# Kernel optimization log

Hardware: AMD Instinct MI355X
Metric: run time of the kernel (lower is better)

The kernel has to match this reference:

```python
import jax, jax.numpy as jnp
from jax import lax
import numpy as np

FEAT = 2048
HID = 512
OUT = 22
B, T = 16, 2048


def _kaiming(key, shape):
    fan_in = shape[1]
    std = np.sqrt(2.0 / fan_in)
    return jax.random.normal(key, shape, dtype=jnp.float32) * std


def setup_inputs() -> dict:
    key = jax.random.key(0)
    ks = jax.random.split(key, 12)
    x = jax.random.normal(ks[0], (B, T, FEAT), dtype=jnp.float32)
    inp = {
        "x": x,
        # main cell (PyTorch LSTMCell gate order: i, f, g, o)
        "w_ih": _kaiming(ks[1], (4 * HID, FEAT)),
        "w_hh": _kaiming(ks[2], (4 * HID, HID)),
        "b_ih": jax.random.uniform(ks[3], (4 * HID,), minval=-0.04, maxval=0.04),
        "b_hh": jax.random.uniform(ks[4], (4 * HID,), minval=-0.04, maxval=0.04),
        # ed cell
        "w_ih_ed": _kaiming(ks[5], (4 * HID, FEAT)),
        "w_hh_ed": _kaiming(ks[6], (4 * HID, HID)),
        "b_ih_ed": jax.random.uniform(ks[7], (4 * HID,), minval=-0.04, maxval=0.04),
        "b_hh_ed": jax.random.uniform(ks[8], (4 * HID,), minval=-0.04, maxval=0.04),
        # linear heads
        "fc_w": _kaiming(ks[9], (OUT, HID)),
        "fc_b": jnp.zeros((OUT,), dtype=jnp.float32),
        "fc_ed_w": _kaiming(ks[10], (OUT, HID)),
        "fc_ed_b": jnp.zeros((OUT,), dtype=jnp.float32),
    }
    return inp


def _run_lstm(x, w_ih, w_hh, b_ih, b_hh):
    # Precompute input projection for all timesteps: [B, T, 4H]
    xg = jnp.einsum("btf,gf->btg", x, w_ih) + (b_ih + b_hh)
    hid = w_hh.shape[1]
    b = x.shape[0]

    def step(carry, xg_t):
        h, c = carry
        g = xg_t + h @ w_hh.T  # [B, 4H]
        i, f, gg, o = jnp.split(g, 4, axis=-1)
        c = jax.nn.sigmoid(f) * c + jax.nn.sigmoid(i) * jnp.tanh(gg)
        h = jax.nn.sigmoid(o) * jnp.tanh(c)
        return (h, c), h

    init = (jnp.zeros((b, hid), x.dtype), jnp.zeros((b, hid), x.dtype))
    _, hs = lax.scan(step, init, jnp.swapaxes(xg, 0, 1))  # hs: [T, B, H]
    return jnp.swapaxes(hs, 0, 1)  # [B, T, H]


def reference(x, w_ih, w_hh, b_ih, b_hh, w_ih_ed, w_hh_ed, b_ih_ed, b_hh_ed,
              fc_w, fc_b, fc_ed_w, fc_ed_b):
    hs = _run_lstm(x, w_ih, w_hh, b_ih, b_hh)
    score = jnp.einsum("bth,oh->bto", hs, fc_w) + fc_b
    hs_ed = _run_lstm(x, w_ih_ed, w_hh_ed, b_ih_ed, b_hh_ed)
    ed = jnp.einsum("bth,oh->bto", hs_ed, fc_ed_w) + fc_ed_b
    return (score, ed)
```

## Files before the change

### kernel.cpp

```cpp
#include <hip/hip_runtime.h>
#include <hip/hip_bf16.h>
#include <stdint.h>

typedef __attribute__((ext_vector_type(8))) short s16x8;
typedef __attribute__((ext_vector_type(4))) float f32x4;
typedef unsigned short u16;
typedef unsigned int u32;
typedef unsigned long long u64;

#define FEAT 2048
#define HID  512
#define GATES 2048
#define NB   16
#define NT   2048
#define NOUT 22
#define MROWS (NB*NT)

#define WS_FLAG 0L
#define WS_BIAS 4096L
#define WS_WF   (WS_BIAS + 16384L)
#define WS_WB   (WS_WF + 4194304L)
#define WS_XB   (WS_WB + 16777216L)
#define WS_XG   (WS_XB + 134217728L)
#define WS_HB   (WS_XG + 268435456L)
#define HB_BYTES 67141632L
#define HB_LSTM_U64 (2049L*2048L)
#define HB_SLAB_U64 2048L

__device__ inline float b2f(u16 u){ u32 x = ((u32)u) << 16; return __builtin_bit_cast(float, x); }
__device__ inline u16 f2b(float f){
  u32 u = __builtin_bit_cast(u32, f);
  u32 r = (u + 0x7FFFu + ((u >> 16) & 1u)) >> 16;
  return (u16)r;
}
__device__ inline float sigm(float x){ return __builtin_amdgcn_rcpf(1.f + __expf(-x)); }
__device__ inline float tanh_(float x){ return 1.f - 2.f*__builtin_amdgcn_rcpf(1.f + __expf(2.f*x)); }

__global__ void detect_dtype(const u32* __restrict__ x, int* __restrict__ flag){
  __shared__ int cs;
  if (threadIdx.x == 0) cs = 0;
  __syncthreads();
  int c = 0;
  for (int i = 0; i < 16; i++){
    u32 w = x[threadIdx.x*16 + i];
    u32 e = (w >> 7) & 0xFFu;
    if ((e >= 110u && e <= 134u) || ((w & 0xFFFFu) == 0u)) c++;
  }
  atomicAdd(&cs, c);
  __syncthreads();
  if (threadIdx.x == 0) *flag = (cs > 2048) ? 1 : 0;
}

__global__ void cvt_bf16(const void* __restrict__ src, u16* __restrict__ dst,
                         long n8, const int* __restrict__ flag){
  const int isb = *flag;
  long stride = (long)gridDim.x * blockDim.x;
  for (long i = (long)blockIdx.x*blockDim.x + threadIdx.x; i < n8; i += stride){
    if (isb){
      ((int4*)dst)[i] = ((const int4*)src)[i];
    } else {
      const float4* s = (const float4*)src + 2*i;
      float4 a = s[0], b = s[1];
      s16x8 o;
      o[0]=(short)f2b(a.x); o[1]=(short)f2b(a.y); o[2]=(short)f2b(a.z); o[3]=(short)f2b(a.w);
      o[4]=(short)f2b(b.x); o[5]=(short)f2b(b.y); o[6]=(short)f2b(b.z); o[7]=(short)f2b(b.w);
      *(s16x8*)(dst + i*8) = o;
    }
  }
}

__global__ void bias_sum(const void* bi0, const void* bh0, const void* bi1, const void* bh1,
                         float* __restrict__ out, const int* __restrict__ flag){
  const int isb = *flag;
  int i = blockIdx.x*256 + threadIdx.x;
  int lstm = i >> 11, idx = i & 2047;
  const void* bi = lstm ? bi1 : bi0;
  const void* bh = lstm ? bh1 : bh0;
  float a = isb ? b2f(((const u16*)bi)[idx]) : ((const float*)bi)[idx];
  float b = isb ? b2f(((const u16*)bh)[idx]) : ((const float*)bh)[idx];
  out[i] = a + b;
}

__global__ void reorder_w(const void* __restrict__ w0, const void* __restrict__ w1,
                          u16* __restrict__ wfr, const int* __restrict__ flag){
  const int isb = *flag;
  int t = blockIdx.x*256 + threadIdx.x;
  int l   = t & 63;
  int kk  = (t >> 6) & 15;
  int tau = (t >> 10) & 127;
  int lstm = t >> 17;
  int m = tau >> 5;
  int w = tau & 31;
  int j = m*512 + w*16 + (l & 15);
  size_t sidx = (size_t)j*HID + kk*32 + (l >> 4)*8;
  const void* src = lstm ? w1 : w0;
  s16x8 o;
  if (isb){
    o = *(const s16x8*)((const u16*)src + sidx);
  } else {
    const float* s = (const float*)src + sidx;
#pragma unroll
    for (int e = 0; e < 8; e++) o[e] = (short)f2b(s[e]);
  }
  *(s16x8*)(wfr + ((((size_t)lstm*128 + tau)*16 + kk)*64 + l)*8) = o;
}

union FSmem {
  struct { u16 As[2][8192]; u16 Bs[2][8192]; } g;
  s16x8 Wl[4][16][64];
  char pad[102400];
};

__global__ __launch_bounds__(256,1) void fused_rec(const u16* __restrict__ wfr,
    const u16* __restrict__ xb, const u16* __restrict__ wb,
    const float* __restrict__ bias, u16* __restrict__ xg, u64* __restrict__ hb64){
  __shared__ FSmem sm;

  if (blockIdx.x >= 64){
    const int gid = blockIdx.x - 64;
    const int lstm = gid & 1;
    const int n0 = ((gid >> 1) & 15) * 128;
    const int y = gid >> 5;
    const int b = y & 15;
    const int tblk = y >> 4;
    const int m0 = b*NT + tblk*128;
    const int tid = threadIdx.x;
    const int lane = tid & 63;
    const int wid = tid >> 6;
    const int wr = wid >> 1, wc = wid & 1;
    const u16* Bw = wb + (size_t)lstm * GATES * FEAT;

    f32x4 acc[4][4] = {};

    auto stage = [&](int buf, int kt){
      const int k0 = kt*64;
#pragma unroll
      for (int i = 0; i < 4; i++){
        int cc = tid + 256*i;
        int row = cc >> 3;
        int slot = cc & 7;
        int slotp = slot ^ (row & 7);
        const u16* ga = xb + (size_t)(m0+row)*FEAT + k0 + slotp*8;
        const u16* gb = Bw + (size_t)(n0+row)*FEAT + k0 + slotp*8;
        __builtin_amdgcn_global_load_lds((const __attribute__((address_space(1))) void*)ga,
            (__attribute__((address_space(3))) void*)&sm.g.As[buf][cc*8], 16, 0, 0);
        __builtin_amdgcn_global_load_lds((const __attribute__((address_space(1))) void*)gb,
            (__attribute__((address_space(3))) void*)&sm.g.Bs[buf][cc*8], 16, 0, 0);
      }
    };

    stage(0, 0);
    __syncthreads();
    for (int kt = 0; kt < 32; kt++){
      int buf = kt & 1;
      if (kt < 31) stage(buf^1, kt+1);
      const char* Ab = (const char*)&sm.g.As[buf][0];
      const char* Bb = (const char*)&sm.g.Bs[buf][0];
#pragma unroll
      for (int ks = 0; ks < 2; ks++){
        s16x8 af[4], bf[4];
#pragma unroll
        for (int mi = 0; mi < 4; mi++){
          int row = wr*64 + mi*16 + (lane & 15);
          int off = row*128 + ((ks*64 + ((lane>>4)*16)) ^ ((row & 7) << 4));
          af[mi] = *(const s16x8*)(Ab + off);
        }
#pragma unroll
        for (int ni = 0; ni < 4; ni++){
          int row = wc*64 + ni*16 + (lane & 15);
          int off = row*128 + ((ks*64 + ((lane>>4)*16)) ^ ((row & 7) << 4));
          bf[ni] = *(const s16x8*)(Bb + off);
        }
#pragma unroll
        for (int mi = 0; mi < 4; mi++)
#pragma unroll
          for (int ni = 0; ni < 4; ni++)
            acc[mi][ni] = __builtin_amdgcn_mfma_f32_16x16x32_bf16(af[mi], bf[ni], acc[mi][ni], 0, 0, 0);
      }
      __syncthreads();
    }

    u16* xgl = xg + (size_t)lstm * MROWS * GATES;
#pragma unroll
    for (int mi = 0; mi < 4; mi++){
#pragma unroll
      for (int ni = 0; ni < 4; ni++){
        int gcol = n0 + wc*64 + ni*16 + (lane & 15);
        float bv = bias[lstm*GATES + gcol];
#pragma unroll
        for (int r = 0; r < 4; r++){
          int grow = m0 + wr*64 + mi*16 + ((lane>>4)<<2) + r;
          u16 val = f2b(acc[mi][ni][r] + bv);
          u16* ad = &xgl[(size_t)grow*GATES + gcol];
          asm volatile("global_store_short %0, %1, off sc0 sc1"
                       :: "v"(ad), "v"((u32)val));
        }
      }
    }
    return;
  }

  if (threadIdx.x >= 64) return;
  const int lstm = blockIdx.x >> 5;
  const int w = blockIdx.x & 31;
  const int lane = threadIdx.x;
  const int n = lane & 15;
  const int g = lane >> 4;
  const int b0 = g * 4;

  u64* myslab = hb64 + (size_t)lstm * HB_LSTM_U64;
  const char* srcp = (const char*)myslab + (size_t)n*1024 + g*16;

  {
    const s16x8* wfb = (const s16x8*)wfr;
#pragma unroll
    for (int tt = 0; tt < 4; tt++){
      const s16x8* wt = wfb + (((size_t)lstm*128 + (tt*32 + w))*16)*64 + lane;
#pragma unroll
      for (int kk = 0; kk < 16; kk++)
        sm.Wl[tt][kk][lane] = wt[kk*64];
    }
  }

  const u16* xpb[4];
#pragma unroll
  for (int m = 0; m < 4; m++)
    xpb[m] = xg + (size_t)lstm*MROWS*GATES + (size_t)b0*NT*GATES + (m*512 + w*16 + n);

  u16 xv[4][4], xn_[4][4];
#pragma unroll
  for (int m = 0; m < 4; m++)
#pragma unroll
    for (int r = 0; r < 4; r++)
      xv[m][r] = xpb[m][(size_t)r*NT*GATES];

  float c[4] = {};

  for (int t = 0; t < NT; t++){
    const size_t tno = (size_t)((t < NT-1) ? (t+1) : t) * GATES;
#pragma unroll
    for (int m = 0; m < 4; m++)
#pragma unroll
      for (int r = 0; r < 4; r++)
        xn_[m][r] = xpb[m][(size_t)r*NT*GATES + tno];

    int4 H0,H1,H2,H3,H4,H5,H6,H7,H8,H9,H10,H11,H12,H13,H14,H15;
    int retry = 0;
    for (;;){
      asm volatile(
        "global_load_dwordx4 %0,  %16, off sc0 sc1\n"
        "global_load_dwordx4 %1,  %16, off offset:64 sc0 sc1\n"
        "global_load_dwordx4 %2,  %16, off offset:128 sc0 sc1\n"
        "global_load_dwordx4 %3,  %16, off offset:192 sc0 sc1\n"
        "global_load_dwordx4 %4,  %16, off offset:256 sc0 sc1\n"
        "global_load_dwordx4 %5,  %16, off offset:320 sc0 sc1\n"
        "global_load_dwordx4 %6,  %16, off offset:384 sc0 sc1\n"
        "global_load_dwordx4 %7,  %16, off offset:448 sc0 sc1\n"
        "global_load_dwordx4 %8,  %16, off offset:512 sc0 sc1\n"
        "global_load_dwordx4 %9,  %16, off offset:576 sc0 sc1\n"
        "global_load_dwordx4 %10, %16, off offset:640 sc0 sc1\n"
        "global_load_dwordx4 %11, %16, off offset:704 sc0 sc1\n"
        "global_load_dwordx4 %12, %16, off offset:768 sc0 sc1\n"
        "global_load_dwordx4 %13, %16, off offset:832 sc0 sc1\n"
        "global_load_dwordx4 %14, %16, off offset:896 sc0 sc1\n"
        "global_load_dwordx4 %15, %16, off offset:960 sc0 sc1\n"
        "s_waitcnt vmcnt(0)"
        : "=v"(H0), "=v"(H1), "=v"(H2), "=v"(H3),
          "=v"(H4), "=v"(H5), "=v"(H6), "=v"(H7),
          "=v"(H8), "=v"(H9), "=v"(H10), "=v"(H11),
          "=v"(H12), "=v"(H13), "=v"(H14), "=v"(H15)
        : "v"(srcp));
      u32 bad = ((u32)H0.x == ~0u) | ((u32)H0.z == ~0u)
              | ((u32)H1.x == ~0u) | ((u32)H1.z == ~0u)
              | ((u32)H2.x == ~0u) | ((u32)H2.z == ~0u)
              | ((u32)H3.x == ~0u) | ((u32)H3.z == ~0u)
              | ((u32)H4.x == ~0u) | ((u32)H4.z == ~0u)
              | ((u32)H5.x == ~0u) | ((u32)H5.z == ~0u)
              | ((u32)H6.x == ~0u) | ((u32)H6.z == ~0u)
              | ((u32)H7.x == ~0u) | ((u32)H7.z == ~0u)
              | ((u32)H8.x == ~0u) | ((u32)H8.z == ~0u)
              | ((u32)H9.x == ~0u) | ((u32)H9.z == ~0u)
              | ((u32)H10.x == ~0u) | ((u32)H10.z == ~0u)
              | ((u32)H11.x == ~0u) | ((u32)H11.z == ~0u)
              | ((u32)H12.x == ~0u) | ((u32)H12.z == ~0u)
              | ((u32)H13.x == ~0u) | ((u32)H13.z == ~0u)
              | ((u32)H14.x == ~0u) | ((u32)H14.z == ~0u)
              | ((u32)H15.x == ~0u) | ((u32)H15.z == ~0u);
      if (!__any(bad)) break;
      retry++;
      if ((retry & 15) == 0){
        int4 F[16];
#pragma unroll
        for (int i = 0; i < 16; i++){
          u64 a = __hip_atomic_load((const u64*)(srcp + i*64),
                                    __ATOMIC_RELAXED, __HIP_MEMORY_SCOPE_AGENT);
          u64 b = __hip_atomic_load((const u64*)(srcp + i*64 + 8),
                                    __ATOMIC_RELAXED, __HIP_MEMORY_SCOPE_AGENT);
          F[i].x = (int)(u32)a; F[i].y = (int)(u32)(a >> 32);
          F[i].z = (int)(u32)b; F[i].w = (int)(u32)(b >> 32);
        }
        u32 bad2 = 0;
#pragma unroll
        for (int i = 0; i < 16; i++)
          bad2 |= ((u32)F[i].x == ~0u) | ((u32)F[i].z == ~0u);
        if (!__any(bad2)){
          H0=F[0]; H1=F[1]; H2=F[2]; H3=F[3]; H4=F[4]; H5=F[5]; H6=F[6]; H7=F[7];
          H8=F[8]; H9=F[9]; H10=F[10]; H11=F[11]; H12=F[12]; H13=F[13]; H14=F[14]; H15=F[15];
          break;
        }
      }
      if (retry > (1 << 15)) break;
      if (retry > 8) __builtin_amdgcn_s_sleep(1);
    }

    {
      u32 xbad = 0;
#pragma unroll
      for (int m = 0; m < 4; m++)
#pragma unroll
        for (int r = 0; r < 4; r++) xbad |= (xv[m][r] == (u16)0xFFFFu);
      if (__builtin_expect(__any(xbad), 0)){
#pragma unroll
        for (int m = 0; m < 4; m++)
#pragma unroll
          for (int r = 0; r < 4; r++){
            if (xv[m][r] == (u16)0xFFFFu){
              const u16* a = xpb[m] + (size_t)r*NT*GATES + (size_t)t*GATES;
              u32 v; int k = 0;
              do {
                asm volatile("global_load_ushort %0, %1, off sc0 sc1\n"
                             "s_waitcnt vmcnt(0)" : "=v"(v) : "v"(a));
              } while ((u16)v == (u16)0xFFFFu && ++k < (1 << 15));
              xv[m][r] = (u16)v;
            }
          }
      }
    }

    f32x4 a0 = {}, a1 = {}, a2 = {}, a3 = {};
#define LMM(kk, HV) { s16x8 hf = __builtin_bit_cast(s16x8, HV); \
      a0 = __builtin_amdgcn_mfma_f32_16x16x32_bf16(hf, sm.Wl[0][kk][lane], a0, 0, 0, 0); \
      a1 = __builtin_amdgcn_mfma_f32_16x16x32_bf16(hf, sm.Wl[1][kk][lane], a1, 0, 0, 0); \
      a2 = __builtin_amdgcn_mfma_f32_16x16x32_bf16(hf, sm.Wl[2][kk][lane], a2, 0, 0, 0); \
      a3 = __builtin_amdgcn_mfma_f32_16x16x32_bf16(hf, sm.Wl[3][kk][lane], a3, 0, 0, 0); }
    LMM(0,H0) LMM(1,H1) LMM(2,H2) LMM(3,H3) LMM(4,H4) LMM(5,H5) LMM(6,H6) LMM(7,H7)
    LMM(8,H8) LMM(9,H9) LMM(10,H10) LMM(11,H11) LMM(12,H12) LMM(13,H13) LMM(14,H14) LMM(15,H15)
#undef LMM

    u16 hob[4];
#pragma unroll
    for (int r = 0; r < 4; r++){
      float iv = a0[r] + b2f(xv[0][r]);
      float fv = a1[r] + b2f(xv[1][r]);
      float gv = a2[r] + b2f(xv[2][r]);
      float ov = a3[r] + b2f(xv[3][r]);
      float cn = sigm(fv)*c[r] + sigm(iv)*tanh_(gv);
      c[r] = cn;
      hob[r] = f2b(sigm(ov)*tanh_(cn));
    }

    u64* dst = myslab + (size_t)(t+1)*HB_SLAB_U64;
    const int base4 = lane & 60;
#pragma unroll
    for (int r = 0; r < 4; r++){
      int hh = (int)hob[r];
      int v0 = __shfl(hh, base4+0, 64) & 0xFFFF;
      int v1 = __shfl(hh, base4+1, 64) & 0xFFFF;
      int v2 = __shfl(hh, base4+2, 64) & 0xFFFF;
      int v3 = __shfl(hh, base4+3, 64) & 0xFFFF;
      u64 v = (u64)(u32)(v0 | (v1 << 16)) | ((u64)(u32)(v2 | (v3 << 16)) << 32);
      if ((lane & 3) == 0){
        u64* d = dst + (size_t)(b0 + r)*128 + (w*4 + (n >> 2));
        __hip_atomic_store(d, v, __ATOMIC_RELAXED, __HIP_MEMORY_SCOPE_AGENT);
      }
    }
#pragma unroll
    for (int m = 0; m < 4; m++)
#pragma unroll
      for (int r = 0; r < 4; r++) xv[m][r] = xn_[m][r];
    srcp += HB_SLAB_U64 * 8;
  }
}

__global__ __launch_bounds__(256,4) void head_fc(const u16* __restrict__ hb,
    const void* fcw0, const void* fcb0, const void* fcw1, const void* fcb1,
    void* __restrict__ dout, const int* __restrict__ flag){
  const int isb = *flag;
  const int lane = threadIdx.x & 63;
  const int wv = threadIdx.x >> 6;
  int row = blockIdx.x*4 + wv;
  const int lstm = row >> 15;
  const int rem = row & 32767;
  const int b = rem >> 11;
  const int t = rem & 2047;
  const u16* hrow = hb + (((size_t)lstm*2049 + (t+1))*16 + b)*512;
  float hv[8];
  {
    s16x8 h8 = *(const s16x8*)(hrow + lane*8);
#pragma unroll
    for (int e = 0; e < 8; e++) hv[e] = b2f((u16)h8[e]);
  }
  const void* fcw = lstm ? fcw1 : fcw0;
  const void* fcb = lstm ? fcb1 : fcb0;
  float bval = 0.f;
  if (lane < NOUT) bval = isb ? b2f(((const u16*)fcb)[lane]) : ((const float*)fcb)[lane];
  float res = 0.f;
  for (int o = 0; o < NOUT; o++){
    float pa = 0.f;
    if (isb){
      s16x8 w8 = *(const s16x8*)((const u16*)fcw + (size_t)o*HID + lane*8);
#pragma unroll
      for (int e = 0; e < 8; e++) pa += hv[e] * b2f((u16)w8[e]);
    } else {
      const float* wr = (const float*)fcw + (size_t)o*HID + lane*8;
#pragma unroll
      for (int e = 0; e < 8; e++) pa += hv[e] * wr[e];
    }
#pragma unroll
    for (int d = 1; d < 64; d <<= 1) pa += __shfl_xor(pa, d, 64);
    if (lane == o) res = pa + bval;
  }
  size_t off = (size_t)lstm*(MROWS*NOUT) + (size_t)rem*NOUT;
  if (lane < NOUT){
    if (isb) ((u16*)dout)[off + lane] = f2b(res);
    else     ((float*)dout)[off + lane] = res;
  }
}

extern "C" void kernel_launch(void* const* d_in, const int* in_sizes, int n_in,
                              void* d_out, int out_size, void* d_ws, size_t ws_size,
                              hipStream_t stream){
  char* ws = (char*)d_ws;
  int*   flag = (int*)(ws + WS_FLAG);
  float* bias = (float*)(ws + WS_BIAS);
  u16*   wfr  = (u16*)(ws + WS_WF);
  u16*   wb   = (u16*)(ws + WS_WB);
  u16*   xb   = (u16*)(ws + WS_XB);
  u16*   xg   = (u16*)(ws + WS_XG);
  u16*   hb   = (u16*)(ws + WS_HB);

  (void)hipMemsetAsync(ws + WS_FLAG, 0, 4096, stream);
  (void)hipMemsetAsync(ws + WS_HB, 0xFF, HB_BYTES, stream);
  (void)hipMemsetAsync(ws + WS_HB, 0, 16384, stream);
  (void)hipMemsetAsync(ws + WS_HB + 2049L*16*512*2, 0, 16384, stream);
  (void)hipMemsetAsync(ws + WS_XG, 0xFF, 268435456L, stream);

  detect_dtype<<<1, 256, 0, stream>>>((const u32*)d_in[0], flag);

  cvt_bf16<<<2048, 256, 0, stream>>>(d_in[0], xb,             67108864L/8, flag);
  cvt_bf16<<<2048, 256, 0, stream>>>(d_in[1], wb,              4194304L/8, flag);
  cvt_bf16<<<2048, 256, 0, stream>>>(d_in[5], wb + 4194304L,   4194304L/8, flag);
  reorder_w<<<1024, 256, 0, stream>>>(d_in[2], d_in[6], wfr, flag);
  bias_sum<<<16, 256, 0, stream>>>(d_in[3], d_in[4], d_in[7], d_in[8], bias, flag);

  fused_rec<<<64 + 8192, 256, 0, stream>>>(wfr, xb, wb, bias, xg, (u64*)hb);
  head_fc<<<16384, 256, 0, stream>>>(hb, d_in[9], d_in[10], d_in[11], d_in[12], d_out, flag);
}
```

Baseline: 8.989 ms.

## Stage xg epilogue through LDS for wide stores; double-buffer atomic h polling

The GEMM epilogue now writes bias-added bf16 results into shared memory and then emits coalesced 16-byte rows to global memory with relaxed agent-scope atomic stores, replacing per-element uncached short stores. The recurrent step's spin-wait for the h slab drops the sleep-and-retry cached-load loop. On a miss it switches to two alternating in-flight buffers of atomic loads, so one poll is always outstanding while the other is checked. This aims to cut epilogue store traffic and the latency between a producer's write and consumer detection, at the cost of more registers and continuous polling without backoff.

```diff
diff --git a/kernel.cpp b/kernel.cpp
--- a/kernel.cpp
+++ b/kernel.cpp
@@ -180,22 +180,32 @@
       __syncthreads();
     }
 
+    u16* Ct = (u16*)&sm.g.As[0][0];
+#pragma unroll
+    for (int mi = 0; mi < 4; mi++){
+#pragma unroll
+      for (int ni = 0; ni < 4; ni++){
+        int ccol = wc*64 + ni*16 + (lane & 15);
+        float bv = bias[lstm*GATES + n0 + ccol];
+#pragma unroll
+        for (int r = 0; r < 4; r++){
+          int crow = wr*64 + mi*16 + ((lane>>4)<<2) + r;
+          Ct[crow*128 + ccol] = f2b(acc[mi][ni][r] + bv);
+        }
+      }
+    }
+    __syncthreads();
     u16* xgl = xg + (size_t)lstm * MROWS * GATES;
 #pragma unroll
-    for (int mi = 0; mi < 4; mi++){
-#pragma unroll
-      for (int ni = 0; ni < 4; ni++){
-        int gcol = n0 + wc*64 + ni*16 + (lane & 15);
-        float bv = bias[lstm*GATES + gcol];
-#pragma unroll
-        for (int r = 0; r < 4; r++){
-          int grow = m0 + wr*64 + mi*16 + ((lane>>4)<<2) + r;
-          u16 val = f2b(acc[mi][ni][r] + bv);
-          u16* ad = &xgl[(size_t)grow*GATES + gcol];
-          asm volatile("global_store_short %0, %1, off sc0 sc1"
-                       :: "v"(ad), "v"((u32)val));
-        }
-      }
+    for (int i = 0; i < 8; i++){
+      int c = tid + 256*i;
+      int row = c >> 4;
+      int sl = c & 15;
+      const u64* lsrc = (const u64*)(Ct + row*128 + sl*8);
+      u64 v0 = lsrc[0], v1 = lsrc[1];
+      u64* ad = (u64*)&xgl[(size_t)(m0+row)*GATES + n0 + sl*8];
+      __hip_atomic_store(ad + 0, v0, __ATOMIC_RELAXED, __HIP_MEMORY_SCOPE_AGENT);
+      __hip_atomic_store(ad + 1, v1, __ATOMIC_RELAXED, __HIP_MEMORY_SCOPE_AGENT);
     }
     return;
   }
@@ -236,6 +246,17 @@
 
   float c[4] = {};
 
+#define MK4(a,b) (int4){(int)(u32)(a), (int)(u32)((a) >> 32), (int)(u32)(b), (int)(u32)((b) >> 32)}
+#define CPYH(S) do { \
+      H0 = MK4(S[0],S[1]);  H1 = MK4(S[2],S[3]);  H2 = MK4(S[4],S[5]);  H3 = MK4(S[6],S[7]); \
+      H4 = MK4(S[8],S[9]);  H5 = MK4(S[10],S[11]);H6 = MK4(S[12],S[13]);H7 = MK4(S[14],S[15]); \
+      H8 = MK4(S[16],S[17]);H9 = MK4(S[18],S[19]);H10= MK4(S[20],S[21]);H11= MK4(S[22],S[23]); \
+      H12= MK4(S[24],S[25]);H13= MK4(S[26],S[27]);H14= MK4(S[28],S[29]);H15= MK4(S[30],S[31]); } while(0)
+#define CISSUE(S) { const u64* sp_ = (const u64*)srcp; \
+      _Pragma("unroll") for (int i = 0; i < 32; i++) \
+        S[i] = __hip_atomic_load(sp_ + ((i >> 1)*8 + (i & 1)), __ATOMIC_RELAXED, __HIP_MEMORY_SCOPE_AGENT); }
+#define CBAD(S,B) { B = 0; _Pragma("unroll") for (int i = 0; i < 32; i++) B |= (S[i] == ~0ULL); }
+
   for (int t = 0; t < NT; t++){
     const size_t tno = (size_t)((t < NT-1) ? (t+1) : t) * GATES;
 #pragma unroll
@@ -245,8 +266,7 @@
         xn_[m][r] = xpb[m][(size_t)r*NT*GATES + tno];
 
     int4 H0,H1,H2,H3,H4,H5,H6,H7,H8,H9,H10,H11,H12,H13,H14,H15;
-    int retry = 0;
-    for (;;){
+    {
       asm volatile(
         "global_load_dwordx4 %0,  %16, off sc0 sc1\n"
         "global_load_dwordx4 %1,  %16, off offset:64 sc0 sc1\n"
@@ -286,31 +306,26 @@
               | ((u32)H13.x == ~0u) | ((u32)H13.z == ~0u)
               | ((u32)H14.x == ~0u) | ((u32)H14.z == ~0u)
               | ((u32)H15.x == ~0u) | ((u32)H15.z == ~0u);
-      if (!__any(bad)) break;
-      retry++;
-      if ((retry & 15) == 0){
-        int4 F[16];
-#pragma unroll
-        for (int i = 0; i < 16; i++){
-          u64 a = __hip_atomic_load((const u64*)(srcp + i*64),
-                                    __ATOMIC_RELAXED, __HIP_MEMORY_SCOPE_AGENT);
-          u64 b = __hip_atomic_load((const u64*)(srcp + i*64 + 8),
-                                    __ATOMIC_RELAXED, __HIP_MEMORY_SCOPE_AGENT);
-          F[i].x = (int)(u32)a; F[i].y = (int)(u32)(a >> 32);
-          F[i].z = (int)(u32)b; F[i].w = (int)(u32)(b >> 32);
+      if (__builtin_expect(__any(bad), 0)){
+        u64 GA[32], GB[32];
+        CISSUE(GA);
+        CISSUE(GB);
+        int useA = 1, rt = 0;
+        for (;;){
+          u32 b2;
+          if (useA){
+            CBAD(GA, b2);
+            if (!__any(b2) || rt > (1 << 15)){ CPYH(GA); break; }
+            CISSUE(GA);
+          } else {
+            CBAD(GB, b2);
+            if (!__any(b2) || rt > (1 << 15)){ CPYH(GB); break; }
+            CISSUE(GB);
+          }
+          useA ^= 1;
+          rt++;
         }
-        u32 bad2 = 0;
-#pragma unroll
-        for (int i = 0; i < 16; i++)
-          bad2 |= ((u32)F[i].x == ~0u) | ((u32)F[i].z == ~0u);
-        if (!__any(bad2)){
-          H0=F[0]; H1=F[1]; H2=F[2]; H3=F[3]; H4=F[4]; H5=F[5]; H6=F[6]; H7=F[7];
-          H8=F[8]; H9=F[9]; H10=F[10]; H11=F[11]; H12=F[12]; H13=F[13]; H14=F[14]; H15=F[15];
-          break;
-        }
-      }
-      if (retry > (1 << 15)) break;
-      if (retry > 8) __builtin_amdgcn_s_sleep(1);
+      }
     }
 
     {
@@ -380,6 +395,10 @@
       for (int r = 0; r < 4; r++) xv[m][r] = xn_[m][r];
     srcp += HB_SLAB_U64 * 8;
   }
+#undef CISSUE
+#undef CBAD
+#undef CPYH
+#undef MK4
 }
 
 __global__ __launch_bounds__(256,4) void head_fc(const u16* __restrict__ hb,
```

Result: slower. 14.69 ms (+63.4%).
